# Performance work log

Measured on AMD Instinct MI355X. Metric: run time of the kernel, lower is better.

The kernel has to match this reference:

```python
import jax, jax.numpy as jnp
import numpy as np
import math

D_MODEL = 1024
HEADS = 16
HEAD_DIM = D_MODEL // HEADS
FFN = 4096
B, S = 2, 2048


def _layer_norm(x, gamma, beta, eps=1e-5):
    mean = jnp.mean(x, axis=-1, keepdims=True)
    var = jnp.mean((x - mean) ** 2, axis=-1, keepdims=True)
    return gamma * (x - mean) / jnp.sqrt(var + eps) + beta


def _sdpa(q, k, v, mask):
    # q,k,v: [B,H,S,dh]; mask: [S,S] additive, broadcasts over B,H
    scaled = jnp.einsum('bhqd,bhkd->bhqk', q, k) / math.sqrt(q.shape[-1])
    scaled = scaled + mask
    attn = jax.nn.softmax(scaled, axis=-1)
    return jnp.einsum('bhqk,bhkd->bhqd', attn, v)


def setup_inputs() -> dict:
    key = jax.random.key(0)
    ks = jax.random.split(key, 12)
    s = 0.02
    inp = {
        'x': jax.random.normal(ks[0], (B, S, D_MODEL), jnp.float32),
        'y': jax.random.normal(ks[1], (B, S, D_MODEL), jnp.float32),
        'self_attention_mask': jnp.zeros((S, S), jnp.float32),
        'cross_attention_mask': jnp.zeros((S, S), jnp.float32),
        # self-attention params
        'Wqkv': jax.random.normal(ks[2], (D_MODEL, 3 * D_MODEL), jnp.float32) * s,
        'bqkv': jnp.zeros((3 * D_MODEL,), jnp.float32),
        'Wo1': jax.random.normal(ks[3], (D_MODEL, D_MODEL), jnp.float32) * s,
        'bo1': jnp.zeros((D_MODEL,), jnp.float32),
        # cross-attention params
        'Wkv': jax.random.normal(ks[4], (D_MODEL, 2 * D_MODEL), jnp.float32) * s,
        'bkv': jnp.zeros((2 * D_MODEL,), jnp.float32),
        'Wq': jax.random.normal(ks[5], (D_MODEL, D_MODEL), jnp.float32) * s,
        'bq': jnp.zeros((D_MODEL,), jnp.float32),
        'Wo2': jax.random.normal(ks[6], (D_MODEL, D_MODEL), jnp.float32) * s,
        'bo2': jnp.zeros((D_MODEL,), jnp.float32),
        # layer norms
        'g1': jnp.ones((D_MODEL,), jnp.float32), 'b1': jnp.zeros((D_MODEL,), jnp.float32),
        'g2': jnp.ones((D_MODEL,), jnp.float32), 'b2': jnp.zeros((D_MODEL,), jnp.float32),
        'g3': jnp.ones((D_MODEL,), jnp.float32), 'b3': jnp.zeros((D_MODEL,), jnp.float32),
        # FFN
        'W1': jax.random.normal(ks[7], (D_MODEL, FFN), jnp.float32) * s,
        'bw1': jnp.zeros((FFN,), jnp.float32),
        'W2': jax.random.normal(ks[8], (FFN, D_MODEL), jnp.float32) * s,
        'bw2': jnp.zeros((D_MODEL,), jnp.float32),
    }
    return inp


def reference(x, y, self_attention_mask, cross_attention_mask,
              Wqkv, bqkv, Wo1, bo1, Wkv, bkv, Wq, bq, Wo2, bo2,
              g1, b1, g2, b2, g3, b3, W1, bw1, W2, bw2):
    b, s, d = y.shape

    # ---- masked self-attention on y ----
    qkv = (y @ Wqkv + bqkv).reshape(b, s, HEADS, 3 * HEAD_DIM).transpose(0, 2, 1, 3)
    q, k, v = jnp.split(qkv, 3, axis=-1)  # each [B,H,S,dh]
    vals = _sdpa(q, k, v, self_attention_mask)
    vals = vals.transpose(0, 2, 1, 3).reshape(b, s, d)
    attn_out = vals @ Wo1 + bo1
    # dropout is identity at inference
    y1 = _layer_norm(attn_out + y, g1, b1)

    # ---- cross attention: q from y1, k/v from x ----
    kv = (x @ Wkv + bkv).reshape(b, s, HEADS, 2 * HEAD_DIM).transpose(0, 2, 1, 3)
    k2, v2 = jnp.split(kv, 2, axis=-1)
    q2 = (y1 @ Wq + bq).reshape(b, s, HEADS, HEAD_DIM).transpose(0, 2, 1, 3)
    vals2 = _sdpa(q2, k2, v2, cross_attention_mask)
    vals2 = vals2.transpose(0, 2, 1, 3).reshape(b, s, d)
    cross_out = vals2 @ Wo2 + bo2
    y2 = _layer_norm(cross_out + y1, g2, b2)

    # ---- FFN ----
    h = jax.nn.relu(y2 @ W1 + bw1)
    ffn_out = h @ W2 + bw2
    y3 = _layer_norm(ffn_out + y2, g3, b3)
    return y3
```

## Files before the change

### kernel.cpp

```cpp
#include <hip/hip_runtime.h>
#include <hip/hip_bf16.h>

#define SEQ      2048
#define BATCH    2
#define DMODEL   1024
#define NHEADS   16
#define HDIM     64
#define FFN_DIM  4096
#define MROWS    (BATCH*SEQ)

typedef __attribute__((ext_vector_type(8))) short bf16x8;
typedef __attribute__((ext_vector_type(4))) float f32x4;

#define GFENCE() asm volatile("" ::: "memory")
#define SBAR()   do { GFENCE(); __builtin_amdgcn_s_barrier(); GFENCE(); } while (0)

__device__ __forceinline__ unsigned short f2b(float f) {
    union { float f; unsigned int u; } v; v.f = f;
    unsigned int u = v.u;
    return (unsigned short)((u + 0x7FFFu + ((u >> 16) & 1u)) >> 16);
}
__device__ __forceinline__ float b2f(unsigned short h) {
    union { unsigned int u; float f; } v; v.u = ((unsigned int)h) << 16;
    return v.f;
}
__device__ __forceinline__ void gload_lds16(const void* g, void* l) {
    __builtin_amdgcn_global_load_lds((const __attribute__((address_space(1))) void*)g,
                                     (__attribute__((address_space(3))) void*)l, 16, 0, 0);
}

__global__ __launch_bounds__(256) void wtrans(const float* __restrict__ W,
                                              unsigned short* __restrict__ Wt,
                                              int K, int N) {
    __shared__ float t[32][33];
    const int n0 = blockIdx.x * 32, k0 = blockIdx.y * 32;
    const int tx = threadIdx.x, ty = threadIdx.y;
#pragma unroll
    for (int i = 0; i < 4; i++)
        t[ty + i * 8][tx] = W[(size_t)(k0 + ty + i * 8) * N + n0 + tx];
    __syncthreads();
#pragma unroll
    for (int i = 0; i < 4; i++) {
        const int n = ty + i * 8;
        Wt[(size_t)(n0 + n) * K + k0 + tx] = f2b(t[tx][n]);
    }
}

__global__ __launch_bounds__(256) void tobf16(const float* __restrict__ in,
                                              unsigned short* __restrict__ out, int n) {
    const int i = (blockIdx.x * 256 + threadIdx.x) * 8;
    if (i >= n) return;
    float4 a = *(const float4*)(in + i);
    float4 b = *(const float4*)(in + i + 4);
    unsigned short r[8] = {f2b(a.x), f2b(a.y), f2b(a.z), f2b(a.w),
                           f2b(b.x), f2b(b.y), f2b(b.z), f2b(b.w)};
    *(uint4*)(out + i) = *(const uint4*)r;
}

template <int RELU, int WF32, int WB16>
__global__ __launch_bounds__(256) void gemm_bt(const unsigned short* __restrict__ A,
                                               const unsigned short* __restrict__ Bt,
                                               const float* __restrict__ bias,
                                               float* __restrict__ Cf,
                                               unsigned short* __restrict__ Cb,
                                               int M, int N, int K) {
    __shared__ __align__(16) unsigned short As[128 * 32];
    __shared__ __align__(16) unsigned short Bs[128 * 32];
    const int tid  = threadIdx.x;
    const int lane = tid & 63;
    const int w    = tid >> 6;
    const int m0   = blockIdx.y << 7;
    const int n0   = blockIdx.x << 7;
    const int wr   = (w >> 1) << 6;
    const int wc   = (w & 1) << 6;
    const int srow = lane >> 2;
    const int scol = (lane & 3) << 3;

    f32x4 acc[4][4];
#pragma unroll
    for (int mi = 0; mi < 4; mi++)
#pragma unroll
        for (int ni = 0; ni < 4; ni++) acc[mi][ni] = (f32x4){0.f, 0.f, 0.f, 0.f};

    for (int k0 = 0; k0 < K; k0 += 32) {
#pragma unroll
        for (int t = 0; t < 2; t++) {
            const int rg  = w * 2 + t;
            const int row = (rg << 4) + srow;
            gload_lds16(A  + (size_t)(m0 + row) * K + k0 + scol, (char*)As + (rg << 10));
            gload_lds16(Bt + (size_t)(n0 + row) * K + k0 + scol, (char*)Bs + (rg << 10));
        }
        __syncthreads();
        const int fr = lane & 15;
        const int fk = (lane >> 4) << 3;
        bf16x8 af[4], bfr[4];
#pragma unroll
        for (int i = 0; i < 4; i++) {
            af[i]  = *(const bf16x8*)(As + (wr + (i << 4) + fr) * 32 + fk);
            bfr[i] = *(const bf16x8*)(Bs + (wc + (i << 4) + fr) * 32 + fk);
        }
#pragma unroll
        for (int mi = 0; mi < 4; mi++)
#pragma unroll
            for (int ni = 0; ni < 4; ni++)
                acc[mi][ni] = __builtin_amdgcn_mfma_f32_16x16x32_bf16(af[mi], bfr[ni], acc[mi][ni], 0, 0, 0);
        __syncthreads();
    }

    const int fr = lane & 15;
    const int fq = lane >> 4;
#pragma unroll
    for (int mi = 0; mi < 4; mi++) {
#pragma unroll
        for (int ni = 0; ni < 4; ni++) {
            const int col = n0 + wc + (ni << 4) + fr;
            const float bv = bias[col];
#pragma unroll
            for (int i = 0; i < 4; i++) {
                const int row = m0 + wr + (mi << 4) + (fq << 2) + i;
                float v = acc[mi][ni][i] + bv;
                if (RELU) v = fmaxf(v, 0.f);
                if (WF32) Cf[(size_t)row * N + col] = v;
                if (WB16) Cb[(size_t)row * N + col] = f2b(v);
            }
        }
    }
}

template <int RELU, int WF32, int WB16>
__global__ __launch_bounds__(512, 2) void gemm256(const unsigned short* __restrict__ A,
                                                  const unsigned short* __restrict__ Bt,
                                                  const float* __restrict__ bias,
                                                  float* __restrict__ Cf,
                                                  unsigned short* __restrict__ Cb,
                                                  int M, int N, int K) {
    __shared__ __align__(16) unsigned short lds[2][2][256 * 64];
    const int tid  = threadIdx.x;
    const int lane = tid & 63;
    const int w    = tid >> 6;
    const int q15  = lane & 15;
    const int g    = lane >> 4;
    const int m0   = blockIdx.y << 8;
    const int n0   = blockIdx.x << 8;
    const int wr   = (w >> 2) << 7;
    const int wc   = (w & 3) << 6;

    f32x4 acc[8][4];
#pragma unroll
    for (int m = 0; m < 8; m++)
#pragma unroll
        for (int n = 0; n < 4; n++) acc[m][n] = (f32x4){0.f, 0.f, 0.f, 0.f};

    const int NT = K >> 6;

    auto stage = [&](int which, int buf, int h, int kt, const unsigned short* src, int base0) {
        char* ldsb = (char*)&lds[buf][which][0];
#pragma unroll
        for (int j = 0; j < 2; j++) {
            const int c    = (w << 7) + (j << 6) + lane;
            const int r    = c >> 3, ci = c & 7;
            const int trow = ((r >> 6) << 7) + (h << 6) + (r & 63);
            const int r0   = (w << 4) + (j << 3);
            const int tr0  = ((r0 >> 6) << 7) + (h << 6) + (r0 & 63);
            gload_lds16(src + (size_t)(base0 + trow) * K + (kt << 6) + ((ci ^ (r & 7)) << 3),
                        ldsb + tr0 * 128);
        }
    };
    auto ldA = [&](int buf, int row, int kc) -> bf16x8 {
        return *(const bf16x8*)((const char*)&lds[buf][0][0] + row * 128 + ((kc ^ (row & 7)) << 4));
    };
    auto ldB = [&](int buf, int row, int kc) -> bf16x8 {
        return *(const bf16x8*)((const char*)&lds[buf][1][0] + row * 128 + ((kc ^ (row & 7)) << 4));
    };

    stage(1, 0, 0, 0, Bt, n0);
    stage(1, 0, 1, 0, Bt, n0);
    stage(0, 0, 0, 0, A, m0);
    stage(0, 0, 1, 0, A, m0);

    for (int t = 0; t < NT; ++t) {
        const int buf = t & 1, nb = buf ^ 1;
        const bool st = (t + 1 < NT);
        bf16x8 bfr[4], af[4];

        if (st) { stage(1, nb, 0, t + 1, Bt, n0);
                  asm volatile("s_waitcnt vmcnt(4)" ::: "memory"); }
        else    { asm volatile("s_waitcnt vmcnt(2)" ::: "memory"); }
        SBAR();
#pragma unroll
        for (int n = 0; n < 4; n++) bfr[n] = ldB(buf, wc + n * 16 + q15, g);
#pragma unroll
        for (int m = 0; m < 4; m++) af[m]  = ldA(buf, wr + m * 16 + q15, g);
        __builtin_amdgcn_s_setprio(1);
#pragma unroll
        for (int m = 0; m < 4; m++)
#pragma unroll
            for (int n = 0; n < 4; n++)
                acc[m][n] = __builtin_amdgcn_mfma_f32_16x16x32_bf16(af[m], bfr[n], acc[m][n], 0, 0, 0);
        __builtin_amdgcn_s_setprio(0);
        SBAR();

        if (st) { stage(1, nb, 1, t + 1, Bt, n0);
                  asm volatile("s_waitcnt vmcnt(4)" ::: "memory"); }
        else    { asm volatile("s_waitcnt vmcnt(0)" ::: "memory"); }
        SBAR();
#pragma unroll
        for (int m = 0; m < 4; m++) af[m] = ldA(buf, wr + 64 + m * 16 + q15, g);
        __builtin_amdgcn_s_setprio(1);
#pragma unroll
        for (int m = 0; m < 4; m++)
#pragma unroll
            for (int n = 0; n < 4; n++)
                acc[4 + m][n] = __builtin_amdgcn_mfma_f32_16x16x32_bf16(af[m], bfr[n], acc[4 + m][n], 0, 0, 0);
        __builtin_amdgcn_s_setprio(0);
        SBAR();

        if (st) stage(0, nb, 0, t + 1, A, m0);
        SBAR();
#pragma unroll
        for (int n = 0; n < 4; n++) bfr[n] = ldB(buf, wc + n * 16 + q15, 4 + g);
#pragma unroll
        for (int m = 0; m < 4; m++) af[m]  = ldA(buf, wr + m * 16 + q15, 4 + g);
        __builtin_amdgcn_s_setprio(1);
#pragma unroll
        for (int m = 0; m < 4; m++)
#pragma unroll
            for (int n = 0; n < 4; n++)
                acc[m][n] = __builtin_amdgcn_mfma_f32_16x16x32_bf16(af[m], bfr[n], acc[m][n], 0, 0, 0);
        __builtin_amdgcn_s_setprio(0);
        SBAR();

        if (st) stage(0, nb, 1, t + 1, A, m0);
        SBAR();
#pragma unroll
        for (int m = 0; m < 4; m++) af[m] = ldA(buf, wr + 64 + m * 16 + q15, 4 + g);
        __builtin_amdgcn_s_setprio(1);
#pragma unroll
        for (int m = 0; m < 4; m++)
#pragma unroll
            for (int n = 0; n < 4; n++)
                acc[4 + m][n] = __builtin_amdgcn_mfma_f32_16x16x32_bf16(af[m], bfr[n], acc[4 + m][n], 0, 0, 0);
        __builtin_amdgcn_s_setprio(0);
        SBAR();
    }

#pragma unroll
    for (int mh = 0; mh < 2; mh++)
#pragma unroll
        for (int mf = 0; mf < 4; mf++)
#pragma unroll
            for (int nf = 0; nf < 4; nf++) {
                const int col = n0 + wc + nf * 16 + q15;
                const float bv = bias[col];
#pragma unroll
                for (int i = 0; i < 4; i++) {
                    const int row = m0 + wr + mh * 64 + mf * 16 + (g << 2) + i;
                    float v = acc[mh * 4 + mf][nf][i] + bv;
                    if (RELU) v = fmaxf(v, 0.f);
                    if (WF32) Cf[(size_t)row * N + col] = v;
                    if (WB16) Cb[(size_t)row * N + col] = f2b(v);
                }
            }
}

template <int WB16>
__global__ __launch_bounds__(256) void resid_ln(const float* __restrict__ xin,
                                                const float* __restrict__ res,
                                                const float* __restrict__ g,
                                                const float* __restrict__ b,
                                                float* __restrict__ outf,
                                                unsigned short* __restrict__ outb) {
    const int row = blockIdx.x;
    const int tid = threadIdx.x;
    const size_t base = (size_t)row * 1024 + tid * 4;
    float4 xv = *(const float4*)(xin + base);
    float4 rv = *(const float4*)(res + base);
    const float v0 = xv.x + rv.x, v1 = xv.y + rv.y, v2 = xv.z + rv.z, v3 = xv.w + rv.w;
    float s  = v0 + v1 + v2 + v3;
    float sq = v0 * v0 + v1 * v1 + v2 * v2 + v3 * v3;
#pragma unroll
    for (int off = 32; off; off >>= 1) { s += __shfl_xor(s, off); sq += __shfl_xor(sq, off); }
    __shared__ float red[8];
    if ((tid & 63) == 0) { red[tid >> 6] = s; red[4 + (tid >> 6)] = sq; }
    __syncthreads();
    s  = red[0] + red[1] + red[2] + red[3];
    sq = red[4] + red[5] + red[6] + red[7];
    const float mean = s * (1.0f / 1024.0f);
    const float var  = sq * (1.0f / 1024.0f) - mean * mean;
    const float inv  = rsqrtf(var + 1e-5f);
    const int col = tid * 4;
    float4 gv = *(const float4*)(g + col);
    float4 bv = *(const float4*)(b + col);
    const float o0 = (v0 - mean) * inv * gv.x + bv.x;
    const float o1 = (v1 - mean) * inv * gv.y + bv.y;
    const float o2 = (v2 - mean) * inv * gv.z + bv.z;
    const float o3 = (v3 - mean) * inv * gv.w + bv.w;
    float4 ov = {o0, o1, o2, o3};
    *(float4*)(outf + base) = ov;
    if (WB16) {
        uint2 u;
        u.x = (unsigned int)f2b(o0) | ((unsigned int)f2b(o1) << 16);
        u.y = (unsigned int)f2b(o2) | ((unsigned int)f2b(o3) << 16);
        *(uint2*)(outb + base) = u;
    }
}

__global__ __launch_bounds__(256) void attn_mfma(
    const unsigned short* __restrict__ Qb, int q_rs, int q_ho,
    const unsigned short* __restrict__ Kb, int k_rs, int k_ho,
    const unsigned short* __restrict__ Vb, int v_rs, int v_ho,
    const float* __restrict__ mask,
    unsigned short* __restrict__ Ob, int o_rs, int o_ho) {
    __shared__ __align__(16) unsigned short Kls[64 * 64];
    __shared__ __align__(16) unsigned short Vraw[64 * 64];
    __shared__ __align__(16) unsigned short QVt[64 * 64];
    __shared__ __align__(16) unsigned short Pls[4][16 * 64];

    const int tid  = threadIdx.x;
    const int lane = tid & 63;
    const int w    = tid >> 6;
    const int g    = lane >> 4;
    const int q15  = lane & 15;
    const int swz  = (lane & 7) << 4;
    const int bh   = blockIdx.y;
    const int b    = bh >> 4, h = bh & 15;
    const int q0   = blockIdx.x << 6;
    const size_t rowbase = (size_t)b * SEQ;

    char* Kc = (char*)Kls;
    char* Vc = (char*)Vraw;
    char* Tc = (char*)QVt;
    char* Pc = (char*)(&Pls[w][0]);

    const int hq = h * q_ho, hk = h * k_ho, hv = h * v_ho;

    auto stage2 = [&](const unsigned short* base, int rs, int hoff, int row0, char* ldsb) {
#pragma unroll
        for (int bb = 0; bb < 2; bb++) {
            const int c = tid + (bb << 8);
            const int r = c >> 3, ci = c & 7;
            gload_lds16(base + (rowbase + row0 + r) * (size_t)rs + hoff + ((ci ^ (r & 7)) << 3),
                        ldsb + ((c >> 6) << 10));
        }
    };

    stage2(Qb, q_rs, hq, q0, Tc);
    stage2(Kb, k_rs, hk, 0, Kc);
    stage2(Vb, v_rs, hv, 0, Vc);

    float m_run = -3.0e38f, l_run = 0.f;
    f32x4 oacc[4];
#pragma unroll
    for (int fd = 0; fd < 4; fd++) oacc[fd] = (f32x4){0.f, 0.f, 0.f, 0.f};

    __syncthreads();
    bf16x8 qf[2];
#pragma unroll
    for (int s = 0; s < 2; s++)
        qf[s] = *(const bf16x8*)(Tc + (w * 16 + q15) * 128 + (((s << 6) + (g << 4)) ^ swz));
    __syncthreads();

    const float* mrow_ptr = mask + (size_t)(q0 + w * 16 + q15) * SEQ;

    for (int t = 0; t < 32; t++) {
        const int kv0 = t << 6;
#pragma unroll
        for (int bb = 0; bb < 2; bb++) {
            const int kvb = bb * 32 + w * 8;
            unsigned short t8[8];
#pragma unroll
            for (int m = 0; m < 8; m++)
                t8[m] = *(const unsigned short*)(Vc + (kvb + m) * 128 + ((2 * lane) ^ (m << 4)));
            *(uint4*)(Tc + lane * 128 + ((2 * kvb) ^ swz)) = *(const uint4*)t8;
        }
        f32x4 sacc[4];
#pragma unroll
        for (int f = 0; f < 4; f++) sacc[f] = (f32x4){0.f, 0.f, 0.f, 0.f};
#pragma unroll
        for (int s = 0; s < 2; s++)
#pragma unroll
            for (int f = 0; f < 4; f++) {
                bf16x8 kf = *(const bf16x8*)(Kc + (f * 16 + q15) * 128 + (((s << 6) + (g << 4)) ^ swz));
                sacc[f] = __builtin_amdgcn_mfma_f32_16x16x32_bf16(kf, qf[s], sacc[f], 0, 0, 0);
            }
        float p[4][4];
        float mt = -3.0e38f;
#pragma unroll
        for (int f = 0; f < 4; f++) {
            float4 mk = *(const float4*)(mrow_ptr + kv0 + f * 16 + g * 4);
            const float* mkp = (const float*)&mk;
#pragma unroll
            for (int r = 0; r < 4; r++) {
                const float v = sacc[f][r] * 0.125f + mkp[r];
                p[f][r] = v;
                mt = fmaxf(mt, v);
            }
        }
        mt = fmaxf(mt, __shfl_xor(mt, 16));
        mt = fmaxf(mt, __shfl_xor(mt, 32));
        const float mnew  = fmaxf(m_run, mt);
        const float alpha = __expf(m_run - mnew);
        m_run = mnew;
        float lsum = 0.f;
#pragma unroll
        for (int f = 0; f < 4; f++)
#pragma unroll
            for (int r = 0; r < 4; r++) {
                const float e = __expf(p[f][r] - mnew);
                p[f][r] = e;
                lsum += e;
            }
        lsum += __shfl_xor(lsum, 16);
        lsum += __shfl_xor(lsum, 32);
        l_run = l_run * alpha + lsum;
#pragma unroll
        for (int f = 0; f < 4; f++) {
            const unsigned int w0 = (unsigned int)f2b(p[f][0]) | ((unsigned int)f2b(p[f][1]) << 16);
            const unsigned int w1 = (unsigned int)f2b(p[f][2]) | ((unsigned int)f2b(p[f][3]) << 16);
            const int bbase = ((f << 5) + (g << 3)) ^ swz;
            *(unsigned int*)(Pc + q15 * 128 + bbase)     = w0;
            *(unsigned int*)(Pc + q15 * 128 + bbase + 4) = w1;
        }
        __syncthreads();
        if (t < 31) {
            stage2(Kb, k_rs, hk, kv0 + 64, Kc);
            stage2(Vb, v_rs, hv, kv0 + 64, Vc);
        }
        float ar[4];
#pragma unroll
        for (int r = 0; r < 4; r++) ar[r] = __shfl(alpha, (g << 4) + (g << 2) + r);
#pragma unroll
        for (int fd = 0; fd < 4; fd++)
#pragma unroll
            for (int r = 0; r < 4; r++) oacc[fd][r] *= ar[r];
#pragma unroll
        for (int s = 0; s < 2; s++) {
            const bf16x8 pf = *(const bf16x8*)(Pc + q15 * 128 + (((s << 6) + (g << 4)) ^ swz));
#pragma unroll
            for (int fd = 0; fd < 4; fd++) {
                const bf16x8 vf = *(const bf16x8*)(Tc + (fd * 16 + q15) * 128 + (((s << 6) + (g << 4)) ^ swz));
                oacc[fd] = __builtin_amdgcn_mfma_f32_16x16x32_bf16(pf, vf, oacc[fd], 0, 0, 0);
            }
        }
        __syncthreads();
    }

    const float rl = 1.0f / l_run;
    float invr[4];
#pragma unroll
    for (int r = 0; r < 4; r++) invr[r] = __shfl(rl, (g << 4) + (g << 2) + r);
    const size_t orow0 = rowbase + q0 + w * 16;
#pragma unroll
    for (int fd = 0; fd < 4; fd++)
#pragma unroll
        for (int r = 0; r < 4; r++) {
            const int qq = (g << 2) + r;
            Ob[(orow0 + qq) * (size_t)o_rs + h * o_ho + fd * 16 + q15] = f2b(oacc[fd][r] * invr[r]);
        }
}

extern "C" void kernel_launch(void* const* d_in, const int* in_sizes, int n_in,
                              void* d_out, int out_size, void* d_ws, size_t ws_size,
                              hipStream_t stream) {
    const float* x     = (const float*)d_in[0];
    const float* y     = (const float*)d_in[1];
    const float* mask1 = (const float*)d_in[2];
    const float* mask2 = (const float*)d_in[3];
    const float* Wqkv  = (const float*)d_in[4];
    const float* bqkv  = (const float*)d_in[5];
    const float* Wo1   = (const float*)d_in[6];
    const float* bo1   = (const float*)d_in[7];
    const float* Wkv   = (const float*)d_in[8];
    const float* bkv   = (const float*)d_in[9];
    const float* Wq    = (const float*)d_in[10];
    const float* bq    = (const float*)d_in[11];
    const float* Wo2   = (const float*)d_in[12];
    const float* bo2   = (const float*)d_in[13];
    const float* g1    = (const float*)d_in[14];
    const float* b1    = (const float*)d_in[15];
    const float* g2    = (const float*)d_in[16];
    const float* b2    = (const float*)d_in[17];
    const float* g3    = (const float*)d_in[18];
    const float* b3    = (const float*)d_in[19];
    const float* W1    = (const float*)d_in[20];
    const float* bw1   = (const float*)d_in[21];
    const float* W2    = (const float*)d_in[22];
    const float* bw2   = (const float*)d_in[23];

    char* ws = (char*)d_ws;
    const size_t o_WqkvT = 0;
    const size_t o_Wo1T  = o_WqkvT + 6291456;
    const size_t o_WkvT  = o_Wo1T  + 2097152;
    const size_t o_WqT   = o_WkvT  + 4194304;
    const size_t o_Wo2T  = o_WqT   + 2097152;
    const size_t o_W1T   = o_Wo2T  + 2097152;
    const size_t o_W2T   = o_W1T   + 8388608;
    const size_t o_xbf   = o_W2T   + 8388608;
    const size_t o_ybf   = o_xbf   + 8388608;
    const size_t o_qkv   = o_ybf   + 8388608;
    const size_t o_vals  = o_qkv   + 25165824;
    const size_t o_tmp   = o_vals  + 8388608;
    const size_t o_y1    = o_tmp   + 16777216;
    const size_t o_y1bf  = o_y1    + 16777216;
    const size_t o_y2    = o_y1bf  + 8388608;
    const size_t o_y2bf  = o_y2    + 16777216;
    const size_t o_kv    = o_qkv;
    const size_t o_q2    = o_qkv + 16777216;
    const size_t o_hbf   = o_xbf;

    unsigned short* pWqkvT = (unsigned short*)(ws + o_WqkvT);
    unsigned short* pWo1T  = (unsigned short*)(ws + o_Wo1T);
    unsigned short* pWkvT  = (unsigned short*)(ws + o_WkvT);
    unsigned short* pWqT   = (unsigned short*)(ws + o_WqT);
    unsigned short* pWo2T  = (unsigned short*)(ws + o_Wo2T);
    unsigned short* pW1T   = (unsigned short*)(ws + o_W1T);
    unsigned short* pW2T   = (unsigned short*)(ws + o_W2T);
    unsigned short* pxbf   = (unsigned short*)(ws + o_xbf);
    unsigned short* pybf   = (unsigned short*)(ws + o_ybf);
    unsigned short* pqkv   = (unsigned short*)(ws + o_qkv);
    unsigned short* pvals  = (unsigned short*)(ws + o_vals);
    float*          ptmp   = (float*)(ws + o_tmp);
    float*          py1    = (float*)(ws + o_y1);
    unsigned short* py1bf  = (unsigned short*)(ws + o_y1bf);
    float*          py2    = (float*)(ws + o_y2);
    unsigned short* py2bf  = (unsigned short*)(ws + o_y2bf);
    unsigned short* pkv    = (unsigned short*)(ws + o_kv);
    unsigned short* pq2    = (unsigned short*)(ws + o_q2);
    unsigned short* phbf   = (unsigned short*)(ws + o_hbf);

    const dim3 tb(32, 8);
    wtrans<<<dim3(3072 / 32, 1024 / 32), tb, 0, stream>>>(Wqkv, pWqkvT, 1024, 3072);
    wtrans<<<dim3(1024 / 32, 1024 / 32), tb, 0, stream>>>(Wo1,  pWo1T,  1024, 1024);
    wtrans<<<dim3(2048 / 32, 1024 / 32), tb, 0, stream>>>(Wkv,  pWkvT,  1024, 2048);
    wtrans<<<dim3(1024 / 32, 1024 / 32), tb, 0, stream>>>(Wq,   pWqT,   1024, 1024);
    wtrans<<<dim3(1024 / 32, 1024 / 32), tb, 0, stream>>>(Wo2,  pWo2T,  1024, 1024);
    wtrans<<<dim3(4096 / 32, 1024 / 32), tb, 0, stream>>>(W1,   pW1T,   1024, 4096);
    wtrans<<<dim3(1024 / 32, 4096 / 32), tb, 0, stream>>>(W2,   pW2T,   4096, 1024);
    tobf16<<<dim3(MROWS * DMODEL / 2048), dim3(256), 0, stream>>>(x, pxbf, MROWS * DMODEL);
    tobf16<<<dim3(MROWS * DMODEL / 2048), dim3(256), 0, stream>>>(y, pybf, MROWS * DMODEL);

    gemm256<0, 0, 1><<<dim3(3072 / 256, MROWS / 256), dim3(512), 0, stream>>>(
        pybf, pWqkvT, bqkv, nullptr, pqkv, MROWS, 3072, 1024);
    attn_mfma<<<dim3(SEQ / 64, BATCH * NHEADS), dim3(256), 0, stream>>>(
        pqkv, 3072, 192, pqkv + 64, 3072, 192, pqkv + 128, 3072, 192,
        mask1, pvals, 1024, 64);
    gemm_bt<0, 1, 0><<<dim3(1024 / 128, MROWS / 128), dim3(256), 0, stream>>>(
        pvals, pWo1T, bo1, ptmp, nullptr, MROWS, 1024, 1024);
    resid_ln<1><<<dim3(MROWS), dim3(256), 0, stream>>>(ptmp, y, g1, b1, py1, py1bf);

    gemm256<0, 0, 1><<<dim3(2048 / 256, MROWS / 256), dim3(512), 0, stream>>>(
        pxbf, pWkvT, bkv, nullptr, pkv, MROWS, 2048, 1024);
    gemm_bt<0, 0, 1><<<dim3(1024 / 128, MROWS / 128), dim3(256), 0, stream>>>(
        py1bf, pWqT, bq, nullptr, pq2, MROWS, 1024, 1024);
    attn_mfma<<<dim3(SEQ / 64, BATCH * NHEADS), dim3(256), 0, stream>>>(
        pq2, 1024, 64, pkv, 2048, 128, pkv + 64, 2048, 128,
        mask2, pvals, 1024, 64);
    gemm_bt<0, 1, 0><<<dim3(1024 / 128, MROWS / 128), dim3(256), 0, stream>>>(
        pvals, pWo2T, bo2, ptmp, nullptr, MROWS, 1024, 1024);
    resid_ln<1><<<dim3(MROWS), dim3(256), 0, stream>>>(ptmp, py1, g2, b2, py2, py2bf);

    gemm256<1, 0, 1><<<dim3(4096 / 256, MROWS / 256), dim3(512), 0, stream>>>(
        py2bf, pW1T, bw1, nullptr, phbf, MROWS, 4096, 1024);
    gemm_bt<0, 1, 0><<<dim3(1024 / 128, MROWS / 128), dim3(256), 0, stream>>>(
        phbf, pW2T, bw2, ptmp, nullptr, MROWS, 1024, 4096);
    resid_ln<0><<<dim3(MROWS), dim3(256), 0, stream>>>(ptmp, py2, g3, b3, (float*)d_out, nullptr);
}
```

Before: 704.2 us.

## Merge prep kernels, widen attention to 128 queries, add lazy softmax rescale

Folds the seven weight-transpose launches and two input casts into a single prep kernel dispatched by block index, which cuts launch overhead. The attention kernel now runs 512 threads over 128 query rows per block, so each staged K/V tile is shared by twice as many queries and the global K/V traffic per query halves. Softmax now updates the running max and rescales the accumulator only when some lane's tile max exceeds the current max by more than 8. The larger block may lower occupancy, and the lazy rescale lets unnormalised exponentials reach up to e^8, which is safe in fp32.

```diff
diff --git a/kernel.cpp b/kernel.cpp
--- a/kernel.cpp
+++ b/kernel.cpp
@@ -29,12 +29,14 @@
                                      (__attribute__((address_space(3))) void*)l, 16, 0, 0);
 }
 
-__global__ __launch_bounds__(256) void wtrans(const float* __restrict__ W,
-                                              unsigned short* __restrict__ Wt,
-                                              int K, int N) {
+__device__ __forceinline__ void trans_tile(const float* __restrict__ W,
+                                           unsigned short* __restrict__ Wt,
+                                           int K, int N, int local) {
     __shared__ float t[32][33];
-    const int n0 = blockIdx.x * 32, k0 = blockIdx.y * 32;
-    const int tx = threadIdx.x, ty = threadIdx.y;
+    const int ntx = N >> 5;
+    const int bx = local % ntx, by = local / ntx;
+    const int n0 = bx * 32, k0 = by * 32;
+    const int tx = threadIdx.x & 31, ty = threadIdx.x >> 5;
 #pragma unroll
     for (int i = 0; i < 4; i++)
         t[ty + i * 8][tx] = W[(size_t)(k0 + ty + i * 8) * N + n0 + tx];
@@ -45,16 +47,33 @@
         Wt[(size_t)(n0 + n) * K + k0 + tx] = f2b(t[tx][n]);
     }
 }
-
-__global__ __launch_bounds__(256) void tobf16(const float* __restrict__ in,
-                                              unsigned short* __restrict__ out, int n) {
-    const int i = (blockIdx.x * 256 + threadIdx.x) * 8;
-    if (i >= n) return;
+__device__ __forceinline__ void cast_blk(const float* __restrict__ in,
+                                         unsigned short* __restrict__ out, int local) {
+    const int i = (local * 256 + threadIdx.x) * 8;
     float4 a = *(const float4*)(in + i);
     float4 b = *(const float4*)(in + i + 4);
     unsigned short r[8] = {f2b(a.x), f2b(a.y), f2b(a.z), f2b(a.w),
                            f2b(b.x), f2b(b.y), f2b(b.z), f2b(b.w)};
     *(uint4*)(out + i) = *(const uint4*)r;
+}
+
+__global__ __launch_bounds__(256) void prep(
+    const float* Wqkv, const float* Wo1, const float* Wkv, const float* Wq,
+    const float* Wo2, const float* W1, const float* W2,
+    const float* x, const float* y,
+    unsigned short* pWqkvT, unsigned short* pWo1T, unsigned short* pWkvT,
+    unsigned short* pWqT, unsigned short* pWo2T, unsigned short* pW1T,
+    unsigned short* pW2T, unsigned short* pxbf, unsigned short* pybf) {
+    const int bid = blockIdx.x;
+    if      (bid < 3072)  trans_tile(Wqkv, pWqkvT, 1024, 3072, bid);
+    else if (bid < 4096)  trans_tile(Wo1,  pWo1T,  1024, 1024, bid - 3072);
+    else if (bid < 6144)  trans_tile(Wkv,  pWkvT,  1024, 2048, bid - 4096);
+    else if (bid < 7168)  trans_tile(Wq,   pWqT,   1024, 1024, bid - 6144);
+    else if (bid < 8192)  trans_tile(Wo2,  pWo2T,  1024, 1024, bid - 7168);
+    else if (bid < 12288) trans_tile(W1,   pW1T,   1024, 4096, bid - 8192);
+    else if (bid < 16384) trans_tile(W2,   pW2T,   4096, 1024, bid - 12288);
+    else if (bid < 18432) cast_blk(x, pxbf, bid - 16384);
+    else                  cast_blk(y, pybf, bid - 18432);
 }
 
 template <int RELU, int WF32, int WB16>
@@ -305,7 +324,7 @@
     }
 }
 
-__global__ __launch_bounds__(256) void attn_mfma(
+__global__ __launch_bounds__(512) void attn_mfma2(
     const unsigned short* __restrict__ Qb, int q_rs, int q_ho,
     const unsigned short* __restrict__ Kb, int k_rs, int k_ho,
     const unsigned short* __restrict__ Vb, int v_rs, int v_ho,
@@ -313,8 +332,8 @@
     unsigned short* __restrict__ Ob, int o_rs, int o_ho) {
     __shared__ __align__(16) unsigned short Kls[64 * 64];
     __shared__ __align__(16) unsigned short Vraw[64 * 64];
-    __shared__ __align__(16) unsigned short QVt[64 * 64];
-    __shared__ __align__(16) unsigned short Pls[4][16 * 64];
+    __shared__ __align__(16) unsigned short QVt[128 * 64];
+    __shared__ __align__(16) unsigned short Pls[8][16 * 64];
 
     const int tid  = threadIdx.x;
     const int lane = tid & 63;
@@ -324,7 +343,7 @@
     const int swz  = (lane & 7) << 4;
     const int bh   = blockIdx.y;
     const int b    = bh >> 4, h = bh & 15;
-    const int q0   = blockIdx.x << 6;
+    const int q0   = blockIdx.x << 7;
     const size_t rowbase = (size_t)b * SEQ;
 
     char* Kc = (char*)Kls;
@@ -334,19 +353,22 @@
 
     const int hq = h * q_ho, hk = h * k_ho, hv = h * v_ho;
 
-    auto stage2 = [&](const unsigned short* base, int rs, int hoff, int row0, char* ldsb) {
-#pragma unroll
-        for (int bb = 0; bb < 2; bb++) {
-            const int c = tid + (bb << 8);
-            const int r = c >> 3, ci = c & 7;
-            gload_lds16(base + (rowbase + row0 + r) * (size_t)rs + hoff + ((ci ^ (r & 7)) << 3),
-                        ldsb + ((c >> 6) << 10));
-        }
+    auto stage64 = [&](const unsigned short* base, int rs, int hoff, int row0, char* ldsb) {
+        const int c = tid;
+        const int r = c >> 3, ci = c & 7;
+        gload_lds16(base + (rowbase + row0 + r) * (size_t)rs + hoff + ((ci ^ (r & 7)) << 3),
+                    ldsb + ((c >> 6) << 10));
     };
 
-    stage2(Qb, q_rs, hq, q0, Tc);
-    stage2(Kb, k_rs, hk, 0, Kc);
-    stage2(Vb, v_rs, hv, 0, Vc);
+#pragma unroll
+    for (int bb = 0; bb < 2; bb++) {
+        const int c = tid + (bb << 9);
+        const int r = c >> 3, ci = c & 7;
+        gload_lds16(Qb + (rowbase + q0 + r) * (size_t)q_rs + hq + ((ci ^ (r & 7)) << 3),
+                    Tc + ((c >> 6) << 10));
+    }
+    stage64(Kb, k_rs, hk, 0, Kc);
+    stage64(Vb, v_rs, hv, 0, Vc);
 
     float m_run = -3.0e38f, l_run = 0.f;
     f32x4 oacc[4];
@@ -364,14 +386,12 @@
 
     for (int t = 0; t < 32; t++) {
         const int kv0 = t << 6;
-#pragma unroll
-        for (int bb = 0; bb < 2; bb++) {
-            const int kvb = bb * 32 + w * 8;
+        {
             unsigned short t8[8];
 #pragma unroll
             for (int m = 0; m < 8; m++)
-                t8[m] = *(const unsigned short*)(Vc + (kvb + m) * 128 + ((2 * lane) ^ (m << 4)));
-            *(uint4*)(Tc + lane * 128 + ((2 * kvb) ^ swz)) = *(const uint4*)t8;
+                t8[m] = *(const unsigned short*)(Vc + (w * 8 + m) * 128 + ((2 * lane) ^ (m << 4)));
+            *(uint4*)(Tc + lane * 128 + ((w << 4) ^ swz)) = *(const uint4*)t8;
         }
         f32x4 sacc[4];
 #pragma unroll
@@ -398,15 +418,19 @@
         }
         mt = fmaxf(mt, __shfl_xor(mt, 16));
         mt = fmaxf(mt, __shfl_xor(mt, 32));
-        const float mnew  = fmaxf(m_run, mt);
-        const float alpha = __expf(m_run - mnew);
-        m_run = mnew;
+        bool rescale = !__all(mt <= m_run + 8.0f);
+        float alpha = 1.0f;
+        if (rescale) {
+            const float mnew = fmaxf(m_run, mt);
+            alpha = __expf(m_run - mnew);
+            m_run = mnew;
+        }
         float lsum = 0.f;
 #pragma unroll
         for (int f = 0; f < 4; f++)
 #pragma unroll
             for (int r = 0; r < 4; r++) {
-                const float e = __expf(p[f][r] - mnew);
+                const float e = __expf(p[f][r] - m_run);
                 p[f][r] = e;
                 lsum += e;
             }
@@ -423,16 +447,18 @@
         }
         __syncthreads();
         if (t < 31) {
-            stage2(Kb, k_rs, hk, kv0 + 64, Kc);
-            stage2(Vb, v_rs, hv, kv0 + 64, Vc);
-        }
-        float ar[4];
-#pragma unroll
-        for (int r = 0; r < 4; r++) ar[r] = __shfl(alpha, (g << 4) + (g << 2) + r);
-#pragma unroll
-        for (int fd = 0; fd < 4; fd++)
-#pragma unroll
-            for (int r = 0; r < 4; r++) oacc[fd][r] *= ar[r];
+            stage64(Kb, k_rs, hk, kv0 + 64, Kc);
+            stage64(Vb, v_rs, hv, kv0 + 64, Vc);
+        }
+        if (rescale) {
+            float ar[4];
+#pragma unroll
+            for (int r = 0; r < 4; r++) ar[r] = __shfl(alpha, (g << 4) + (g << 2) + r);
+#pragma unroll
+            for (int fd = 0; fd < 4; fd++)
+#pragma unroll
+                for (int r = 0; r < 4; r++) oacc[fd][r] *= ar[r];
+        }
 #pragma unroll
         for (int s = 0; s < 2; s++) {
             const bf16x8 pf = *(const bf16x8*)(Pc + q15 * 128 + (((s << 6) + (g << 4)) ^ swz));
@@ -528,20 +554,13 @@
     unsigned short* pq2    = (unsigned short*)(ws + o_q2);
     unsigned short* phbf   = (unsigned short*)(ws + o_hbf);
 
-    const dim3 tb(32, 8);
-    wtrans<<<dim3(3072 / 32, 1024 / 32), tb, 0, stream>>>(Wqkv, pWqkvT, 1024, 3072);
-    wtrans<<<dim3(1024 / 32, 1024 / 32), tb, 0, stream>>>(Wo1,  pWo1T,  1024, 1024);
-    wtrans<<<dim3(2048 / 32, 1024 / 32), tb, 0, stream>>>(Wkv,  pWkvT,  1024, 2048);
-    wtrans<<<dim3(1024 / 32, 1024 / 32), tb, 0, stream>>>(Wq,   pWqT,   1024, 1024);
-    wtrans<<<dim3(1024 / 32, 1024 / 32), tb, 0, stream>>>(Wo2,  pWo2T,  1024, 1024);
-    wtrans<<<dim3(4096 / 32, 1024 / 32), tb, 0, stream>>>(W1,   pW1T,   1024, 4096);
-    wtrans<<<dim3(1024 / 32, 4096 / 32), tb, 0, stream>>>(W2,   pW2T,   4096, 1024);
-    tobf16<<<dim3(MROWS * DMODEL / 2048), dim3(256), 0, stream>>>(x, pxbf, MROWS * DMODEL);
-    tobf16<<<dim3(MROWS * DMODEL / 2048), dim3(256), 0, stream>>>(y, pybf, MROWS * DMODEL);
+    prep<<<dim3(20480), dim3(256), 0, stream>>>(Wqkv, Wo1, Wkv, Wq, Wo2, W1, W2, x, y,
+                                                pWqkvT, pWo1T, pWkvT, pWqT, pWo2T,
+                                                pW1T, pW2T, pxbf, pybf);
 
     gemm256<0, 0, 1><<<dim3(3072 / 256, MROWS / 256), dim3(512), 0, stream>>>(
         pybf, pWqkvT, bqkv, nullptr, pqkv, MROWS, 3072, 1024);
-    attn_mfma<<<dim3(SEQ / 64, BATCH * NHEADS), dim3(256), 0, stream>>>(
+    attn_mfma2<<<dim3(SEQ / 128, BATCH * NHEADS), dim3(512), 0, stream>>>(
         pqkv, 3072, 192, pqkv + 64, 3072, 192, pqkv + 128, 3072, 192,
         mask1, pvals, 1024, 64);
     gemm_bt<0, 1, 0><<<dim3(1024 / 128, MROWS / 128), dim3(256), 0, stream>>>(
@@ -552,7 +571,7 @@
         pxbf, pWkvT, bkv, nullptr, pkv, MROWS, 2048, 1024);
     gemm_bt<0, 0, 1><<<dim3(1024 / 128, MROWS / 128), dim3(256), 0, stream>>>(
         py1bf, pWqT, bq, nullptr, pq2, MROWS, 1024, 1024);
-    attn_mfma<<<dim3(SEQ / 64, BATCH * NHEADS), dim3(256), 0, stream>>>(
+    attn_mfma2<<<dim3(SEQ / 128, BATCH * NHEADS), dim3(512), 0, stream>>>(
         pq2, 1024, 64, pkv, 2048, 128, pkv + 64, 2048, 128,
         mask2, pvals, 1024, 64);
     gemm_bt<0, 1, 0><<<dim3(1024 / 128, MROWS / 128), dim3(256), 0, stream>>>(
```

After: 709.2 us. No clear change (+0.7%).
